# Performance work log

Hardware: AMD Instinct MI355X
Metric: run time of the kernel (lower is better)

Reference implementation:

```python
import jax, jax.numpy as jnp
import numpy as np

N, T = 32, 1024
CIN, H, O, F2 = 64, 128, 16, 16  # F2 = 2 * FiLMed_layers
EPS = 1e-5
SLOPE = 0.01  # nn.LeakyReLU default


def _leaky(x):
    return jnp.where(x >= 0, x, SLOPE * x)


def _ln(x, gamma, beta):
    # x: (N,T,O,H); gamma,beta: (O,H) -> broadcast per channel
    mu = jnp.mean(x, axis=-1, keepdims=True)
    var = jnp.mean(jnp.square(x - mu), axis=-1, keepdims=True)
    return (x - mu) * jax.lax.rsqrt(var + EPS) * gamma + beta


def setup_inputs() -> dict:
    key = jax.random.key(0)
    ks = jax.random.split(key, 7)
    s0 = 1.0 / np.sqrt(CIN)
    s1 = 1.0 / np.sqrt(H)
    return {
        "x": jax.random.normal(ks[0], (N, T, CIN), jnp.float32),
        "W0": jax.random.uniform(ks[1], (O, H, CIN), jnp.float32, -s0, s0),
        "b0": jax.random.uniform(ks[2], (O, H), jnp.float32, -s0, s0),
        "g0": jnp.ones((O, H), jnp.float32),
        "be0": jnp.zeros((O, H), jnp.float32),
        "W1": jax.random.uniform(ks[3], (O, H, H), jnp.float32, -s1, s1),
        "b1": jax.random.uniform(ks[4], (O, H), jnp.float32, -s1, s1),
        "g1": jnp.ones((O, H), jnp.float32),
        "be1": jnp.zeros((O, H), jnp.float32),
        "W2": jax.random.uniform(ks[5], (O, F2, H), jnp.float32, -s1, s1),
        "b2": jax.random.uniform(ks[6], (O, F2), jnp.float32, -s1, s1),
    }


def reference(x, W0, b0, g0, be0, W1, b1, g1, be1, W2, b2):
    # Per-channel MLP, vectorized over the O channel axis.
    h = jnp.einsum("ntc,ohc->ntoh", x, W0) + b0          # (N,T,O,H)
    h = _ln(_leaky(h), g0, be0)
    h = jnp.einsum("ntoh,ogh->ntog", h, W1) + b1         # (N,T,O,H)
    h = _ln(_leaky(h), g1, be1)
    out = jnp.einsum("ntoh,ofh->ntof", h, W2) + b2       # (N,T,O,F2)
    out = _leaky(out)
    # torch: stack(dim=1) -> (N,O,T,F2); moveaxis(1,-1) -> (N,T,F2,O)
    return jnp.moveaxis(out, 2, 3)
```

## Files before the change

### kernel.cpp

```cpp
#include <hip/hip_runtime.h>
#include <hip/hip_bf16.h>

#define NTOK  32768
#define CIN   64
#define HDIM  128
#define O_CH  16
#define F2    16
#define SLOPE 0.01f
#define EPS   1e-5f

#define SW0_STRIDE 72
#define SW1_STRIDE 136
#define SW2_STRIDE 136
#define SH_STRIDE  136
#define SW0_OFF 0
#define SW1_OFF 9216
#define SW2_OFF (9216 + 17408)
#define WIMG_SHORTS 28800
#define SH_OFF  28800
#define SH_ROWS 256
#define SBIAS_OFF (SH_OFF + SH_ROWS * SH_STRIDE)
#define SBIAS_FLOATS 272
#define SMEM_SHORTS (SBIAS_OFF + SBIAS_FLOATS * 2)

#define WIMG_OFF   0
#define WIMG_BYTES ((size_t)O_CH * WIMG_SHORTS * 2)
#define B0F_OFF    WIMG_BYTES
#define B0F_BYTES  ((size_t)O_CH * HDIM * 4)
#define B1F_OFF    (B0F_OFF + B0F_BYTES)
#define B1F_BYTES  ((size_t)O_CH * HDIM * 4)
#define B2F_OFF    (B1F_OFF + B1F_BYTES)

typedef __attribute__((ext_vector_type(8))) short bf16x8;
typedef __attribute__((ext_vector_type(4))) short bf16x4;
typedef __attribute__((ext_vector_type(4))) float f32x4;

__device__ __forceinline__ unsigned short f2b(float f) {
  union { float f; unsigned int i; } v;
  v.f = f;
  unsigned int i = v.i;
  unsigned int r = (i + 0x7fffu + ((i >> 16) & 1u)) >> 16;
  return (unsigned short)r;
}
__device__ __forceinline__ short f2bn(float f) {
  union { __hip_bfloat16 h; short s; } v;
  v.h = __float2bfloat16(f);
  return v.s;
}
__device__ __forceinline__ float leaky(float t) {
  return fmaxf(t, SLOPE * t);
}
__device__ __forceinline__ bf16x8 cvt8(const float* __restrict__ p) {
  float4 a = *(const float4*)p;
  float4 b = *(const float4*)(p + 4);
  bf16x8 r;
  r[0] = (short)f2b(a.x); r[1] = (short)f2b(a.y);
  r[2] = (short)f2b(a.z); r[3] = (short)f2b(a.w);
  r[4] = (short)f2b(b.x); r[5] = (short)f2b(b.y);
  r[6] = (short)f2b(b.z); r[7] = (short)f2b(b.w);
  return r;
}
__device__ __forceinline__ bf16x8 cvt8s(const float* __restrict__ p,
                                        const float* __restrict__ s) {
  bf16x8 r;
#pragma unroll
  for (int i = 0; i < 8; ++i) r[i] = (short)f2b(p[i] * s[i]);
  return r;
}

__device__ __forceinline__ void leaky_ln_store(
    f32x4* acc, unsigned short* __restrict__ sh,
    int row0, int lo16, int quad) {
  float s1 = 0.f, s2 = 0.f;
#pragma unroll
  for (int nt = 0; nt < 8; ++nt) {
#pragma unroll
    for (int r = 0; r < 4; ++r) {
      float t = leaky(acc[nt][r]);
      acc[nt][r] = t;
      s1 += t;
      s2 += t * t;
    }
  }
  s1 += __shfl_xor(s1, 16); s2 += __shfl_xor(s2, 16);
  s1 += __shfl_xor(s1, 32); s2 += __shfl_xor(s2, 32);
  float mu = s1 * (1.0f / 128.0f);
  float var = s2 * (1.0f / 128.0f) - mu * mu;
  float rs = rsqrtf(var + EPS);
  float nm = -mu * rs;
  unsigned short* dst = sh + (row0 + lo16) * SH_STRIDE + quad * 4;
#pragma unroll
  for (int nt = 0; nt < 8; ++nt) {
    bf16x4 p;
    p[0] = f2bn(fmaf(acc[nt][0], rs, nm));
    p[1] = f2bn(fmaf(acc[nt][1], rs, nm));
    p[2] = f2bn(fmaf(acc[nt][2], rs, nm));
    p[3] = f2bn(fmaf(acc[nt][3], rs, nm));
    *(bf16x4*)(dst + nt * 16) = p;
  }
}

__global__ __launch_bounds__(256) void prep(
    const float* __restrict__ W0, const float* __restrict__ b0,
    const float* __restrict__ g0, const float* __restrict__ be0,
    const float* __restrict__ W1, const float* __restrict__ b1,
    const float* __restrict__ g1, const float* __restrict__ be1,
    const float* __restrict__ W2, const float* __restrict__ b2,
    unsigned short* __restrict__ wimg,
    float* __restrict__ b0f, float* __restrict__ b1f,
    float* __restrict__ b2f) {
  const int o = blockIdx.x, tid = threadIdx.x;
  __shared__ float sg0[HDIM], sbe0[HDIM], sg1[HDIM], sbe1[HDIM];
  if (tid < 128) {
    sg0[tid]  = g0 [o * HDIM + tid];
    sbe0[tid] = be0[o * HDIM + tid];
    sg1[tid]  = g1 [o * HDIM + tid];
    sbe1[tid] = be1[o * HDIM + tid];
  }
  __syncthreads();
  unsigned short* img = wimg + (size_t)o * WIMG_SHORTS;
  const float* w0 = W0 + (size_t)o * HDIM * CIN;
  for (int c = tid; c < (HDIM * CIN) / 8; c += 256) {
    int n = c >> 3, k8 = c & 7;
    *(bf16x8*)&img[SW0_OFF + n * SW0_STRIDE + k8 * 8] = cvt8(w0 + c * 8);
  }
  const float* w1 = W1 + (size_t)o * HDIM * HDIM;
  for (int c = tid; c < (HDIM * HDIM) / 8; c += 256) {
    int n = c >> 4, k8 = c & 15;
    *(bf16x8*)&img[SW1_OFF + n * SW1_STRIDE + k8 * 8] =
        cvt8s(w1 + c * 8, sg0 + k8 * 8);
  }
  const float* w2 = W2 + (size_t)o * F2 * HDIM;
  for (int c = tid; c < (F2 * HDIM) / 8; c += 256) {
    int n = c >> 4, k8 = c & 15;
    *(bf16x8*)&img[SW2_OFF + n * SW2_STRIDE + k8 * 8] =
        cvt8s(w2 + c * 8, sg1 + k8 * 8);
  }
  if (tid < 128) {
    b0f[o * HDIM + tid] = b0[o * HDIM + tid];
    float d = 0.f;
    const float* w1r = w1 + (size_t)tid * HDIM;
    for (int k = 0; k < HDIM; ++k) d += w1r[k] * sbe0[k];
    b1f[o * HDIM + tid] = b1[o * HDIM + tid] + d;
  } else if (tid < 144) {
    int f = tid - 128;
    float d = 0.f;
    const float* w2r = w2 + (size_t)f * HDIM;
    for (int k = 0; k < HDIM; ++k) d += w2r[k] * sbe1[k];
    b2f[o * F2 + f] = b2[o * F2 + f] + d;
  }
}

__global__ __launch_bounds__(1024)
__attribute__((amdgpu_waves_per_eu(4, 4))) void film_main(
    const float* __restrict__ x,
    const unsigned short* __restrict__ wimg,
    const float* __restrict__ b0f, const float* __restrict__ b1f,
    const float* __restrict__ b2f,
    float* __restrict__ out) {
  __shared__ unsigned short smem[SMEM_SHORTS];
  const int tid = threadIdx.x;
  const int c   = blockIdx.x & 7;
  const int o   = (blockIdx.x >> 3) & 15;
  const int q   = blockIdx.x >> 7;
  const int tok0 = (q * 8 + c) * 1024;

  {
    const bf16x8* src = (const bf16x8*)(wimg + (size_t)o * WIMG_SHORTS);
    for (int i = tid; i < WIMG_SHORTS / 8; i += 1024)
      *(bf16x8*)&smem[i * 8] = src[i];
  }
  float* sbias = (float*)&smem[SBIAS_OFF];
  if (tid < 128)      sbias[tid] = b0f[o * HDIM + tid];
  else if (tid < 256) sbias[tid] = b1f[o * HDIM + (tid - 128)];
  else if (tid < 272) sbias[tid] = b2f[o * F2 + (tid - 256)];

  const int lane = tid & 63;
  const int wave = tid >> 6;
  const int lo16 = lane & 15;
  const int quad = lane >> 4;
  const int row0 = wave * 16;
  const float* sb0 = sbias;
  const float* sb1 = sbias + HDIM;
  const float* sb2 = sbias + 2 * HDIM;
  __syncthreads();

  for (int mt = 0; mt < 4; ++mt) {
    const int trow = tok0 + wave * 64 + mt * 16;

    f32x4 acc[8];
#pragma unroll
    for (int nt = 0; nt < 8; ++nt)
      acc[nt] = *(const f32x4*)(sb0 + nt * 16 + quad * 4);
    {
      const float* xr = x + (size_t)(trow + lo16) * CIN + quad * 8;
#pragma unroll
      for (int ks = 0; ks < 2; ++ks) {
        float4 xa = *(const float4*)(xr + ks * 32);
        float4 xb = *(const float4*)(xr + ks * 32 + 4);
        bf16x8 bx;
        bx[0] = f2bn(xa.x); bx[1] = f2bn(xa.y);
        bx[2] = f2bn(xa.z); bx[3] = f2bn(xa.w);
        bx[4] = f2bn(xb.x); bx[5] = f2bn(xb.y);
        bx[6] = f2bn(xb.z); bx[7] = f2bn(xb.w);
#pragma unroll
        for (int nt = 0; nt < 8; ++nt) {
          bf16x8 a = *(const bf16x8*)
              &smem[SW0_OFF + (nt * 16 + lo16) * SW0_STRIDE + ks * 32 + quad * 8];
          acc[nt] = __builtin_amdgcn_mfma_f32_16x16x32_bf16(a, bx, acc[nt], 0, 0, 0);
        }
      }
    }
    leaky_ln_store(acc, smem + SH_OFF, row0, lo16, quad);

#pragma unroll
    for (int nt = 0; nt < 8; ++nt)
      acc[nt] = *(const f32x4*)(sb1 + nt * 16 + quad * 4);
#pragma unroll
    for (int ks = 0; ks < 4; ++ks) {
      bf16x8 bh = *(const bf16x8*)
          &smem[SH_OFF + (row0 + lo16) * SH_STRIDE + ks * 32 + quad * 8];
#pragma unroll
      for (int nt = 0; nt < 8; ++nt) {
        bf16x8 a = *(const bf16x8*)
            &smem[SW1_OFF + (nt * 16 + lo16) * SW1_STRIDE + ks * 32 + quad * 8];
        acc[nt] = __builtin_amdgcn_mfma_f32_16x16x32_bf16(a, bh, acc[nt], 0, 0, 0);
      }
    }
    leaky_ln_store(acc, smem + SH_OFF, row0, lo16, quad);

    f32x4 acc2 = *(const f32x4*)(sb2 + quad * 4);
#pragma unroll
    for (int ks = 0; ks < 4; ++ks) {
      bf16x8 bh = *(const bf16x8*)
          &smem[SH_OFF + (row0 + lo16) * SH_STRIDE + ks * 32 + quad * 8];
      bf16x8 a = *(const bf16x8*)
          &smem[SW2_OFF + lo16 * SW2_STRIDE + ks * 32 + quad * 8];
      acc2 = __builtin_amdgcn_mfma_f32_16x16x32_bf16(a, bh, acc2, 0, 0, 0);
    }
    {
      const size_t tb = (size_t)(trow + lo16) * (F2 * O_CH);
#pragma unroll
      for (int r = 0; r < 4; ++r)
        out[tb + (quad * 4 + r) * O_CH + o] = leaky(acc2[r]);
    }
  }
}

extern "C" void kernel_launch(void* const* d_in, const int* in_sizes, int n_in,
                              void* d_out, int out_size, void* d_ws, size_t ws_size,
                              hipStream_t stream) {
  (void)in_sizes; (void)n_in; (void)out_size; (void)ws_size;
  const float* x   = (const float*)d_in[0];
  const float* W0  = (const float*)d_in[1];
  const float* b0  = (const float*)d_in[2];
  const float* g0  = (const float*)d_in[3];
  const float* be0 = (const float*)d_in[4];
  const float* W1  = (const float*)d_in[5];
  const float* b1  = (const float*)d_in[6];
  const float* g1  = (const float*)d_in[7];
  const float* be1 = (const float*)d_in[8];
  const float* W2  = (const float*)d_in[9];
  const float* b2  = (const float*)d_in[10];

  unsigned short* wimg = (unsigned short*)((char*)d_ws + WIMG_OFF);
  float* b0f = (float*)((char*)d_ws + B0F_OFF);
  float* b1f = (float*)((char*)d_ws + B1F_OFF);
  float* b2f = (float*)((char*)d_ws + B2F_OFF);

  prep<<<dim3(O_CH), dim3(256), 0, stream>>>(
      W0, b0, g0, be0, W1, b1, g1, be1, W2, b2, wimg, b0f, b1f, b2f);
  film_main<<<dim3(O_CH * (NTOK / 1024)), dim3(1024), 0, stream>>>(
      x, wimg, b0f, b1f, b2f, (float*)d_out);
}
```

Baseline: 151.1 us.

## Pass activations between layers via register shuffles instead of LDS round-trip

Replaces the shared-memory staging of normalized hidden activations with packed bf16 registers that are redistributed into MFMA B-operand layout using cross-lane shuffles. This removes the LDS store/load traffic for the hidden tile and shrinks shared memory to just weights and biases, which could allow more blocks per CU. The waves_per_eu attribute is dropped and LN sums use split accumulators. In exchange it adds many ds_bpermute shuffles per k-step and raises register pressure.

```diff
diff --git a/kernel.cpp b/kernel.cpp
--- a/kernel.cpp
+++ b/kernel.cpp
@@ -12,14 +12,11 @@
 #define SW0_STRIDE 72
 #define SW1_STRIDE 136
 #define SW2_STRIDE 136
-#define SH_STRIDE  136
 #define SW0_OFF 0
 #define SW1_OFF 9216
 #define SW2_OFF (9216 + 17408)
 #define WIMG_SHORTS 28800
-#define SH_OFF  28800
-#define SH_ROWS 256
-#define SBIAS_OFF (SH_OFF + SH_ROWS * SH_STRIDE)
+#define SBIAS_OFF WIMG_SHORTS
 #define SBIAS_FLOATS 272
 #define SMEM_SHORTS (SBIAS_OFF + SBIAS_FLOATS * 2)
 
@@ -42,8 +39,8 @@
   unsigned int r = (i + 0x7fffu + ((i >> 16) & 1u)) >> 16;
   return (unsigned short)r;
 }
-__device__ __forceinline__ short f2bn(float f) {
-  union { __hip_bfloat16 h; short s; } v;
+__device__ __forceinline__ unsigned short f2bn(float f) {
+  union { __hip_bfloat16 h; unsigned short s; } v;
   v.h = __float2bfloat16(f);
   return v.s;
 }
@@ -68,36 +65,55 @@
   return r;
 }
 
-__device__ __forceinline__ void leaky_ln_store(
-    f32x4* acc, unsigned short* __restrict__ sh,
-    int row0, int lo16, int quad) {
-  float s1 = 0.f, s2 = 0.f;
+__device__ __forceinline__ void leaky_ln_pack(
+    f32x4* acc, unsigned* pk01, unsigned* pk23) {
+  float a0 = 0.f, a1 = 0.f, a2 = 0.f, a3 = 0.f;
+  float c0 = 0.f, c1 = 0.f, c2 = 0.f, c3 = 0.f;
 #pragma unroll
   for (int nt = 0; nt < 8; ++nt) {
-#pragma unroll
-    for (int r = 0; r < 4; ++r) {
-      float t = leaky(acc[nt][r]);
-      acc[nt][r] = t;
-      s1 += t;
-      s2 += t * t;
-    }
-  }
+    float t0 = leaky(acc[nt][0]);
+    float t1 = leaky(acc[nt][1]);
+    float t2 = leaky(acc[nt][2]);
+    float t3 = leaky(acc[nt][3]);
+    acc[nt][0] = t0; acc[nt][1] = t1; acc[nt][2] = t2; acc[nt][3] = t3;
+    a0 += t0; a1 += t1; a2 += t2; a3 += t3;
+    c0 = fmaf(t0, t0, c0); c1 = fmaf(t1, t1, c1);
+    c2 = fmaf(t2, t2, c2); c3 = fmaf(t3, t3, c3);
+  }
+  float s1 = (a0 + a1) + (a2 + a3);
+  float s2 = (c0 + c1) + (c2 + c3);
   s1 += __shfl_xor(s1, 16); s2 += __shfl_xor(s2, 16);
   s1 += __shfl_xor(s1, 32); s2 += __shfl_xor(s2, 32);
   float mu = s1 * (1.0f / 128.0f);
   float var = s2 * (1.0f / 128.0f) - mu * mu;
   float rs = rsqrtf(var + EPS);
   float nm = -mu * rs;
-  unsigned short* dst = sh + (row0 + lo16) * SH_STRIDE + quad * 4;
 #pragma unroll
   for (int nt = 0; nt < 8; ++nt) {
-    bf16x4 p;
-    p[0] = f2bn(fmaf(acc[nt][0], rs, nm));
-    p[1] = f2bn(fmaf(acc[nt][1], rs, nm));
-    p[2] = f2bn(fmaf(acc[nt][2], rs, nm));
-    p[3] = f2bn(fmaf(acc[nt][3], rs, nm));
-    *(bf16x4*)(dst + nt * 16) = p;
-  }
+    unsigned lo0 = f2bn(fmaf(acc[nt][0], rs, nm));
+    unsigned hi0 = f2bn(fmaf(acc[nt][1], rs, nm));
+    unsigned lo1 = f2bn(fmaf(acc[nt][2], rs, nm));
+    unsigned hi1 = f2bn(fmaf(acc[nt][3], rs, nm));
+    pk01[nt] = lo0 | (hi0 << 16);
+    pk23[nt] = lo1 | (hi1 << 16);
+  }
+}
+
+__device__ __forceinline__ bf16x8 build_bh(
+    const unsigned* pk01, const unsigned* pk23, int e, int o,
+    int srcA, int srcB, bool hi32) {
+  unsigned e01 = pk01[e], o01 = pk01[o];
+  unsigned e23 = pk23[e], o23 = pk23[o];
+  unsigned s1a = __shfl(e01, srcA, 64), s2a = __shfl(o01, srcA, 64);
+  unsigned s3a = __shfl(e23, srcA, 64), s4a = __shfl(o23, srcA, 64);
+  unsigned s1b = __shfl(e01, srcB, 64), s2b = __shfl(o01, srcB, 64);
+  unsigned s3b = __shfl(e23, srcB, 64), s4b = __shfl(o23, srcB, 64);
+  union { unsigned w[4]; bf16x8 v; } bh;
+  bh.w[0] = hi32 ? s2a : s1a;
+  bh.w[1] = hi32 ? s4a : s3a;
+  bh.w[2] = hi32 ? s2b : s1b;
+  bh.w[3] = hi32 ? s4b : s3b;
+  return bh.v;
 }
 
 __global__ __launch_bounds__(256) void prep(
@@ -151,8 +167,7 @@
   }
 }
 
-__global__ __launch_bounds__(1024)
-__attribute__((amdgpu_waves_per_eu(4, 4))) void film_main(
+__global__ __launch_bounds__(1024) void film_main(
     const float* __restrict__ x,
     const unsigned short* __restrict__ wimg,
     const float* __restrict__ b0f, const float* __restrict__ b1f,
@@ -179,7 +194,9 @@
   const int wave = tid >> 6;
   const int lo16 = lane & 15;
   const int quad = lane >> 4;
-  const int row0 = wave * 16;
+  const bool hi32 = (lane & 32) != 0;
+  const int srcA = lo16 + ((quad & 1) << 5);
+  const int srcB = srcA + 16;
   const float* sb0 = sbias;
   const float* sb1 = sbias + HDIM;
   const float* sb2 = sbias + 2 * HDIM;
@@ -187,6 +204,7 @@
 
   for (int mt = 0; mt < 4; ++mt) {
     const int trow = tok0 + wave * 64 + mt * 16;
+    unsigned pk01[8], pk23[8];
 
     f32x4 acc[8];
 #pragma unroll
@@ -199,10 +217,10 @@
         float4 xa = *(const float4*)(xr + ks * 32);
         float4 xb = *(const float4*)(xr + ks * 32 + 4);
         bf16x8 bx;
-        bx[0] = f2bn(xa.x); bx[1] = f2bn(xa.y);
-        bx[2] = f2bn(xa.z); bx[3] = f2bn(xa.w);
-        bx[4] = f2bn(xb.x); bx[5] = f2bn(xb.y);
-        bx[6] = f2bn(xb.z); bx[7] = f2bn(xb.w);
+        bx[0] = (short)f2bn(xa.x); bx[1] = (short)f2bn(xa.y);
+        bx[2] = (short)f2bn(xa.z); bx[3] = (short)f2bn(xa.w);
+        bx[4] = (short)f2bn(xb.x); bx[5] = (short)f2bn(xb.y);
+        bx[6] = (short)f2bn(xb.z); bx[7] = (short)f2bn(xb.w);
 #pragma unroll
         for (int nt = 0; nt < 8; ++nt) {
           bf16x8 a = *(const bf16x8*)
@@ -211,15 +229,14 @@
         }
       }
     }
-    leaky_ln_store(acc, smem + SH_OFF, row0, lo16, quad);
+    leaky_ln_pack(acc, pk01, pk23);
 
 #pragma unroll
     for (int nt = 0; nt < 8; ++nt)
       acc[nt] = *(const f32x4*)(sb1 + nt * 16 + quad * 4);
 #pragma unroll
     for (int ks = 0; ks < 4; ++ks) {
-      bf16x8 bh = *(const bf16x8*)
-          &smem[SH_OFF + (row0 + lo16) * SH_STRIDE + ks * 32 + quad * 8];
+      bf16x8 bh = build_bh(pk01, pk23, 2 * ks, 2 * ks + 1, srcA, srcB, hi32);
 #pragma unroll
       for (int nt = 0; nt < 8; ++nt) {
         bf16x8 a = *(const bf16x8*)
@@ -227,13 +244,12 @@
         acc[nt] = __builtin_amdgcn_mfma_f32_16x16x32_bf16(a, bh, acc[nt], 0, 0, 0);
       }
     }
-    leaky_ln_store(acc, smem + SH_OFF, row0, lo16, quad);
+    leaky_ln_pack(acc, pk01, pk23);
 
     f32x4 acc2 = *(const f32x4*)(sb2 + quad * 4);
 #pragma unroll
     for (int ks = 0; ks < 4; ++ks) {
-      bf16x8 bh = *(const bf16x8*)
-          &smem[SH_OFF + (row0 + lo16) * SH_STRIDE + ks * 32 + quad * 8];
+      bf16x8 bh = build_bh(pk01, pk23, 2 * ks, 2 * ks + 1, srcA, srcB, hi32);
       bf16x8 a = *(const bf16x8*)
           &smem[SW2_OFF + lo16 * SW2_STRIDE + ks * 32 + quad * 8];
       acc2 = __builtin_amdgcn_mfma_f32_16x16x32_bf16(a, bh, acc2, 0, 0, 0);
```

Measured after the change: 579.5 us. +283.4%, slower.
